# Kernel tuning notes

Measured on AMD Instinct MI355X. Metric: run time of the kernel, lower is better.

The kernel has to match this reference:

```python
import jax, jax.numpy as jnp
import numpy as np

NEG_INF = -9e15  # matches torch's -9000000000000000.0 mask value
ALPHA = 0.2      # leakyrelu slope for attention scores
OUT_SLOPE = 0.01 # default F.leaky_relu slope on the output


def setup_inputs() -> dict:
    key = jax.random.key(0)
    k = jax.random.split(key, 6)
    B, Ns, Nt = 4, 4096, 4096
    Fs, Ft, Fo = 256, 256, 64
    h = jax.random.normal(k[0], (B, Nt, Ft), dtype=jnp.float32)
    ctx = jax.random.normal(k[1], (B, Ns, Fs), dtype=jnp.float32)
    adj = jax.random.randint(k[2], (B, Nt, Ns), 0, 2, dtype=jnp.int32)
    Ws = jax.random.normal(k[3], (Fs, Fo), dtype=jnp.float32) * (1.414 * (6.0 / (Fs + Fo)) ** 0.5)
    Wt = jax.random.normal(k[4], (Ft, Fo), dtype=jnp.float32) * (1.414 * (6.0 / (Ft + Fo)) ** 0.5)
    a = jax.random.normal(k[5], (2 * Fo, 1), dtype=jnp.float32) * (1.414 * (6.0 / (2 * Fo + 1)) ** 0.5)
    return {"h": h, "ctx": ctx, "adj": adj, "Ws": Ws, "Wt": Wt, "a": a}


def _leaky(x, slope):
    return jnp.where(x > 0, x, slope * x)


def reference(h, ctx, adj, Ws, Wt, a):
    Fo = Ws.shape[1]
    Ws_ctx = jnp.einsum('bsf,fo->bso', ctx, Ws)   # [B, Ns, Fo]
    Wt_h = jnp.einsum('btf,fo->bto', h, Wt)       # [B, Nt, Fo]
    B, Ns, _ = Ws_ctx.shape
    Nt = Wt_h.shape[1]
    # a_input @ a decomposes: score(i,j) = Ws_ctx[i]@a[:Fo] + Wt_h[j]@a[Fo:]
    s = Ws_ctx @ a[:Fo, 0]  # [B, Ns]
    t = Wt_h @ a[Fo:, 0]    # [B, Nt]
    # Original builds flat order i*Nt + j (i over Ns, j over Nt), then views as [B, Nt, Ns].
    raw = s[:, :, None] + t[:, None, :]           # [B, Ns, Nt], flat index i*Nt+j
    e = _leaky(raw, ALPHA).reshape(B, Nt, Ns)     # faithful reshape
    masked = jnp.where(adj > 0, e, jnp.full_like(e, NEG_INF))
    attn = jax.nn.softmax(masked, axis=2)         # [B, Nt, Ns]
    h_prime = jnp.einsum('bts,bso->bto', attn, Ws_ctx)
    return _leaky(h_prime, OUT_SLOPE)
```

## Files before the change

### kernel.cpp

```cpp
#include <hip/hip_runtime.h>

#define BB 4
#define NS 4096
#define NT 4096
#define FS 256
#define FT 256
#define FO 64
#define ALPHA 0.2f
#define OUT_SLOPE 0.01f
#define JSPLIT 4

typedef __attribute__((ext_vector_type(8))) short short8;
typedef __attribute__((ext_vector_type(4))) float floatx4;

__device__ __forceinline__ float leaky(float x, float s) { return x > 0.f ? x : s * x; }
__device__ __forceinline__ float leaky_max(float x, float s) { return fmaxf(x, s * x); }

__device__ __forceinline__ short f2bf(float x) {
  union { float f; unsigned u; } c; c.f = x;
  unsigned r = c.u + 0x7fffu + ((c.u >> 16) & 1u);
  return (short)(r >> 16);
}

__global__ void k_wa(const float* __restrict__ Wt, const float* __restrict__ a,
                     float* __restrict__ wa) {
  int f = threadIdx.x;
  float acc = 0.f;
#pragma unroll
  for (int o = 0; o < FO; ++o) acc += Wt[f * FO + o] * a[FO + o];
  wa[f] = acc;
}

__global__ __launch_bounds__(256) void k_t(const float* __restrict__ h,
                                           const float* __restrict__ wa,
                                           float* __restrict__ tvec) {
  int lane = threadIdx.x & 63, wave = threadIdx.x >> 6;
  int row = blockIdx.x * 4 + wave;
  const float4* hp = (const float4*)(h + (size_t)row * FT);
  const float4* wp = (const float4*)wa;
  float4 hv = hp[lane], wv = wp[lane];
  float acc = hv.x * wv.x + hv.y * wv.y + hv.z * wv.z + hv.w * wv.w;
#pragma unroll
  for (int off = 32; off; off >>= 1) acc += __shfl_down(acc, off);
  if (lane == 0) tvec[row] = acc;
}

__global__ __launch_bounds__(256) void k_tmax(const float* __restrict__ tvec,
                                              float* __restrict__ tmax) {
  __shared__ float red[256];
  int b = blockIdx.x, tid = threadIdx.x;
  float m = -3.0e38f;
  for (int j = tid; j < NS; j += 256) m = fmaxf(m, tvec[b * NS + j]);
  red[tid] = m;
  __syncthreads();
  for (int s = 128; s; s >>= 1) {
    if (tid < s) red[tid] = fmaxf(red[tid], red[tid + s]);
    __syncthreads();
  }
  if (tid == 0) tmax[b] = red[0];
}

__global__ __launch_bounds__(256) void k_wsctx(const float* __restrict__ ctx,
                                               const float* __restrict__ Ws,
                                               const float* __restrict__ a,
                                               short* __restrict__ vT,
                                               float* __restrict__ svec) {
  const int f = threadIdx.x & 63, wave = threadIdx.x >> 6;
  const int row0 = blockIdx.x * 16 + wave * 4;
  const float4* c0 = (const float4*)(ctx + (size_t)(row0 + 0) * FS);
  const float4* c1 = (const float4*)(ctx + (size_t)(row0 + 1) * FS);
  const float4* c2 = (const float4*)(ctx + (size_t)(row0 + 2) * FS);
  const float4* c3 = (const float4*)(ctx + (size_t)(row0 + 3) * FS);
  float r0 = 0.f, r1 = 0.f, r2 = 0.f, r3 = 0.f;
#pragma unroll 2
  for (int k4 = 0; k4 < FS / 4; ++k4) {
    const float w0 = Ws[(k4 * 4 + 0) * FO + f];
    const float w1 = Ws[(k4 * 4 + 1) * FO + f];
    const float w2 = Ws[(k4 * 4 + 2) * FO + f];
    const float w3 = Ws[(k4 * 4 + 3) * FO + f];
    float4 x;
    x = c0[k4]; r0 += x.x * w0 + x.y * w1 + x.z * w2 + x.w * w3;
    x = c1[k4]; r1 += x.x * w0 + x.y * w1 + x.z * w2 + x.w * w3;
    x = c2[k4]; r2 += x.x * w0 + x.y * w1 + x.z * w2 + x.w * w3;
    x = c3[k4]; r3 += x.x * w0 + x.y * w1 + x.z * w2 + x.w * w3;
  }
  const int b = row0 >> 12;
  const int rloc = row0 & (NS - 1);
  short* vp = vT + ((size_t)b * FO + f) * NS + rloc;
  vp[0] = f2bf(r0); vp[1] = f2bf(r1); vp[2] = f2bf(r2); vp[3] = f2bf(r3);

  const float af = a[f];
  float s0 = r0 * af, s1 = r1 * af, s2 = r2 * af, s3 = r3 * af;
#pragma unroll
  for (int off = 32; off; off >>= 1) {
    s0 += __shfl_down(s0, off);
    s1 += __shfl_down(s1, off);
    s2 += __shfl_down(s2, off);
    s3 += __shfl_down(s3, off);
  }
  if (f == 0) {
    svec[row0 + 0] = s0;
    svec[row0 + 1] = s1;
    svec[row0 + 2] = s2;
    svec[row0 + 3] = s3;
  }
}

__global__ __launch_bounds__(256) void k_part(const int* __restrict__ adj,
                                              const short* __restrict__ vT,
                                              const float* __restrict__ svec,
                                              const float* __restrict__ tvec,
                                              const float* __restrict__ tmax,
                                              float* __restrict__ outpart,
                                              float* __restrict__ lpart) {
  const int lane = threadIdx.x & 63;
  const int wv = threadIdx.x >> 6;
  const int m = lane & 15;
  const int q = lane >> 4;

  const int tile = blockIdx.x >> 2;
  const int js = blockIdx.x & (JSPLIT - 1);
  const int b = tile >> 6;
  const int i0 = (tile & 63) * 64;
  const int jbase = js * (NS / JSPLIT);

  const int r = i0 + wv * 16 + m;
  const float sr = svec[b * NS + r];
  const float cr = leaky_max(sr + tmax[b], ALPHA);

  const int* arow = adj + ((size_t)(b * NT) + r) * NS + jbase;
  const float* tp = tvec + b * NS + jbase;
  const short* vp0 = vT + ((size_t)b * FO + m) * NS + jbase;

  floatx4 acc0 = {0.f, 0.f, 0.f, 0.f};
  floatx4 acc1 = {0.f, 0.f, 0.f, 0.f};
  floatx4 acc2 = {0.f, 0.f, 0.f, 0.f};
  floatx4 acc3 = {0.f, 0.f, 0.f, 0.f};
  float lsum = 0.f;

#pragma unroll 2
  for (int jc = 0; jc < (NS / JSPLIT) / 32; ++jc) {
    const int j0 = jc * 32 + q * 8;
    const int4 a0 = *(const int4*)(arow + j0);
    const int4 a1 = *(const int4*)(arow + j0 + 4);
    const float4 t0 = *(const float4*)(tp + j0);
    const float4 t1 = *(const float4*)(tp + j0 + 4);

    float w[8];
    w[0] = (a0.x > 0) ? __expf(leaky_max(sr + t0.x, ALPHA) - cr) : 0.f;
    w[1] = (a0.y > 0) ? __expf(leaky_max(sr + t0.y, ALPHA) - cr) : 0.f;
    w[2] = (a0.z > 0) ? __expf(leaky_max(sr + t0.z, ALPHA) - cr) : 0.f;
    w[3] = (a0.w > 0) ? __expf(leaky_max(sr + t0.w, ALPHA) - cr) : 0.f;
    w[4] = (a1.x > 0) ? __expf(leaky_max(sr + t1.x, ALPHA) - cr) : 0.f;
    w[5] = (a1.y > 0) ? __expf(leaky_max(sr + t1.y, ALPHA) - cr) : 0.f;
    w[6] = (a1.z > 0) ? __expf(leaky_max(sr + t1.z, ALPHA) - cr) : 0.f;
    w[7] = (a1.w > 0) ? __expf(leaky_max(sr + t1.w, ALPHA) - cr) : 0.f;

    lsum += ((w[0] + w[1]) + (w[2] + w[3])) + ((w[4] + w[5]) + (w[6] + w[7]));

    short8 af;
#pragma unroll
    for (int i = 0; i < 8; ++i) af[i] = f2bf(w[i]);

    const short8 bf0 = *(const short8*)(vp0 + 0 * 16 * NS + j0);
    const short8 bf1 = *(const short8*)(vp0 + 1 * 16 * NS + j0);
    const short8 bf2 = *(const short8*)(vp0 + 2 * 16 * NS + j0);
    const short8 bf3 = *(const short8*)(vp0 + 3 * 16 * NS + j0);
    acc0 = __builtin_amdgcn_mfma_f32_16x16x32_bf16(af, bf0, acc0, 0, 0, 0);
    acc1 = __builtin_amdgcn_mfma_f32_16x16x32_bf16(af, bf1, acc1, 0, 0, 0);
    acc2 = __builtin_amdgcn_mfma_f32_16x16x32_bf16(af, bf2, acc2, 0, 0, 0);
    acc3 = __builtin_amdgcn_mfma_f32_16x16x32_bf16(af, bf3, acc3, 0, 0, 0);
  }

  float v = lsum;
  v += __shfl_down(v, 32);
  v += __shfl_down(v, 16);
  if (lane < 16) lpart[(size_t)js * BB * NT + (size_t)b * NT + i0 + wv * 16 + m] = v;

  float* op = outpart + (size_t)js * BB * NT * FO +
              ((size_t)(b * NT) + i0 + wv * 16 + q * 4) * FO + m;
#pragma unroll
  for (int reg = 0; reg < 4; ++reg) {
    op[(size_t)reg * FO + 0 * 16] = acc0[reg];
    op[(size_t)reg * FO + 1 * 16] = acc1[reg];
    op[(size_t)reg * FO + 2 * 16] = acc2[reg];
    op[(size_t)reg * FO + 3 * 16] = acc3[reg];
  }
}

__global__ __launch_bounds__(256) void k_fin(const float* __restrict__ outpart,
                                             const float* __restrict__ lpart,
                                             float* __restrict__ out) {
  const size_t NP = (size_t)BB * NT * FO;
  const int idx = blockIdx.x * 256 + threadIdx.x;
  const int row = idx >> 4;
  float l = lpart[row] + lpart[BB * NT + row] + lpart[2 * BB * NT + row] +
            lpart[3 * BB * NT + row];
  const float inv = 1.f / l;
  float4 v0 = ((const float4*)(outpart + 0 * NP))[idx];
  float4 v1 = ((const float4*)(outpart + 1 * NP))[idx];
  float4 v2 = ((const float4*)(outpart + 2 * NP))[idx];
  float4 v3 = ((const float4*)(outpart + 3 * NP))[idx];
  float4 o;
  o.x = leaky_max((v0.x + v1.x + v2.x + v3.x) * inv, OUT_SLOPE);
  o.y = leaky_max((v0.y + v1.y + v2.y + v3.y) * inv, OUT_SLOPE);
  o.z = leaky_max((v0.z + v1.z + v2.z + v3.z) * inv, OUT_SLOPE);
  o.w = leaky_max((v0.w + v1.w + v2.w + v3.w) * inv, OUT_SLOPE);
  ((float4*)out)[idx] = o;
}

extern "C" void kernel_launch(void* const* d_in, const int* in_sizes, int n_in,
                              void* d_out, int out_size, void* d_ws, size_t ws_size,
                              hipStream_t stream) {
  const float* h   = (const float*)d_in[0];
  const float* ctx = (const float*)d_in[1];
  const int*   adj = (const int*)d_in[2];
  const float* Ws  = (const float*)d_in[3];
  const float* Wt  = (const float*)d_in[4];
  const float* a   = (const float*)d_in[5];
  float* out = (float*)d_out;
  float* ws = (float*)d_ws;

  float* outpart = ws;
  float* lpart   = outpart + (size_t)JSPLIT * BB * NT * FO;
  float* tvec    = lpart + (size_t)JSPLIT * BB * NT;
  float* svec    = tvec + BB * NS;
  float* wa      = svec + BB * NS;
  float* tmax    = wa + 256;
  short* vT      = (short*)(tmax + 4);

  k_wa<<<1, 256, 0, stream>>>(Wt, a, wa);
  k_t<<<(BB * NT) / 4, 256, 0, stream>>>(h, wa, tvec);
  k_tmax<<<BB, 256, 0, stream>>>(tvec, tmax);
  k_wsctx<<<(BB * NS) / 16, 256, 0, stream>>>(ctx, Ws, a, vT, svec);
  k_part<<<(BB * NT / 64) * JSPLIT, 256, 0, stream>>>(adj, vT, svec, tvec, tmax,
                                                      outpart, lpart);
  k_fin<<<(BB * NT * FO / 4) / 256, 256, 0, stream>>>(outpart, lpart, out);
}
```

Baseline: 486.0 us.

## Fuse Wt·a and t-vector kernels, use nontemporal adj loads, unroll main loop more

Merges the single-block wa kernel and the per-row t kernel into one launch. Each block recomputes Wt·a into shared memory and then handles 64 rows, which removes one launch and a global round trip for wa. In the main partial kernel, adj is now read with nontemporal loads to avoid polluting the cache with streamed data, and the j loop unroll goes from 2 to 4. The costs are redundant Wt·a work in every block and higher register pressure from the larger unroll.

```diff
diff --git a/kernel.cpp b/kernel.cpp
--- a/kernel.cpp
+++ b/kernel.cpp
@@ -12,8 +12,8 @@
 
 typedef __attribute__((ext_vector_type(8))) short short8;
 typedef __attribute__((ext_vector_type(4))) float floatx4;
-
-__device__ __forceinline__ float leaky(float x, float s) { return x > 0.f ? x : s * x; }
+typedef __attribute__((ext_vector_type(4))) int int4v;
+
 __device__ __forceinline__ float leaky_max(float x, float s) { return fmaxf(x, s * x); }
 
 __device__ __forceinline__ short f2bf(float x) {
@@ -22,27 +22,30 @@
   return (short)(r >> 16);
 }
 
-__global__ void k_wa(const float* __restrict__ Wt, const float* __restrict__ a,
-                     float* __restrict__ wa) {
-  int f = threadIdx.x;
-  float acc = 0.f;
-#pragma unroll
-  for (int o = 0; o < FO; ++o) acc += Wt[f * FO + o] * a[FO + o];
-  wa[f] = acc;
-}
-
-__global__ __launch_bounds__(256) void k_t(const float* __restrict__ h,
-                                           const float* __restrict__ wa,
-                                           float* __restrict__ tvec) {
-  int lane = threadIdx.x & 63, wave = threadIdx.x >> 6;
-  int row = blockIdx.x * 4 + wave;
-  const float4* hp = (const float4*)(h + (size_t)row * FT);
-  const float4* wp = (const float4*)wa;
-  float4 hv = hp[lane], wv = wp[lane];
-  float acc = hv.x * wv.x + hv.y * wv.y + hv.z * wv.z + hv.w * wv.w;
-#pragma unroll
-  for (int off = 32; off; off >>= 1) acc += __shfl_down(acc, off);
-  if (lane == 0) tvec[row] = acc;
+__global__ __launch_bounds__(256) void k_pre(const float* __restrict__ Wt,
+                                             const float* __restrict__ a,
+                                             const float* __restrict__ h,
+                                             float* __restrict__ tvec) {
+  __shared__ __align__(16) float wa[256];
+  const int tid = threadIdx.x;
+  {
+    float acc = 0.f;
+#pragma unroll 8
+    for (int o = 0; o < FO; ++o) acc += Wt[tid * FO + o] * a[FO + o];
+    wa[tid] = acc;
+  }
+  __syncthreads();
+  const int lane = tid & 63, wv = tid >> 6;
+  const float4 w4 = ((const float4*)wa)[lane];
+#pragma unroll 4
+  for (int rr = 0; rr < 16; ++rr) {
+    const int row = blockIdx.x * 64 + wv * 16 + rr;
+    const float4 hv = ((const float4*)(h + (size_t)row * FT))[lane];
+    float acc = hv.x * w4.x + hv.y * w4.y + hv.z * w4.z + hv.w * w4.w;
+#pragma unroll
+    for (int off = 32; off; off >>= 1) acc += __shfl_down(acc, off);
+    if (lane == 0) tvec[row] = acc;
+  }
 }
 
 __global__ __launch_bounds__(256) void k_tmax(const float* __restrict__ tvec,
@@ -138,11 +141,11 @@
   floatx4 acc3 = {0.f, 0.f, 0.f, 0.f};
   float lsum = 0.f;
 
-#pragma unroll 2
+#pragma unroll 4
   for (int jc = 0; jc < (NS / JSPLIT) / 32; ++jc) {
     const int j0 = jc * 32 + q * 8;
-    const int4 a0 = *(const int4*)(arow + j0);
-    const int4 a1 = *(const int4*)(arow + j0 + 4);
+    const int4v a0 = __builtin_nontemporal_load((const int4v*)(arow + j0));
+    const int4v a1 = __builtin_nontemporal_load((const int4v*)(arow + j0 + 4));
     const float4 t0 = *(const float4*)(tp + j0);
     const float4 t1 = *(const float4*)(tp + j0 + 4);
 
@@ -225,12 +228,10 @@
   float* lpart   = outpart + (size_t)JSPLIT * BB * NT * FO;
   float* tvec    = lpart + (size_t)JSPLIT * BB * NT;
   float* svec    = tvec + BB * NS;
-  float* wa      = svec + BB * NS;
-  float* tmax    = wa + 256;
+  float* tmax    = svec + BB * NS;
   short* vT      = (short*)(tmax + 4);
 
-  k_wa<<<1, 256, 0, stream>>>(Wt, a, wa);
-  k_t<<<(BB * NT) / 4, 256, 0, stream>>>(h, wa, tvec);
+  k_pre<<<(BB * NT) / 64, 256, 0, stream>>>(Wt, a, h, tvec);
   k_tmax<<<BB, 256, 0, stream>>>(tvec, tmax);
   k_wsctx<<<(BB * NS) / 16, 256, 0, stream>>>(ctx, Ws, a, vT, svec);
   k_part<<<(BB * NT / 64) * JSPLIT, 256, 0, stream>>>(adj, vT, svec, tvec, tmax,
```

New measurement: 516.1 us. 6.2% more time.
